# Kernel tuning notes

Hardware: AMD Instinct MI355X
Metric: run time of the kernel (lower is better)

## Reference

```python
import jax, jax.numpy as jnp
import numpy as np

VOCAB, EDIM, WFEAT, LABELS, SLOPE = 50000, 128, 128, 2, 0.01
N = 8192

def setup_inputs() -> dict:
    key = jax.random.key(0)
    ks = jax.random.split(key, 8)
    inSen = jax.random.randint(ks[0], (N,), 0, VOCAB, dtype=jnp.int64) if jax.config.read('jax_enable_x64') else jax.random.randint(ks[0], (N,), 0, VOCAB, dtype=jnp.int32)
    adj = jax.random.randint(ks[1], (N, N), 0, 2, dtype=jnp.int32)
    emb = jax.random.normal(ks[2], (VOCAB, EDIM), dtype=jnp.float32)
    W = jax.random.normal(ks[3], (EDIM, WFEAT), dtype=jnp.float32) * (1.0 / np.sqrt(EDIM))
    a_src = jax.random.normal(ks[4], (WFEAT,), dtype=jnp.float32) * (1.0 / np.sqrt(WFEAT))
    a_dst = jax.random.normal(ks[5], (WFEAT,), dtype=jnp.float32) * (1.0 / np.sqrt(WFEAT))
    cls_W = jax.random.normal(ks[6], (WFEAT, LABELS), dtype=jnp.float32) * (1.0 / np.sqrt(WFEAT))
    cls_b = jax.random.normal(ks[7], (LABELS,), dtype=jnp.float32) * 0.01
    return {"inSen": inSen, "adj": adj, "selfLink": 1, "emb": emb, "W": W,
            "a_src": a_src, "a_dst": a_dst, "cls_W": cls_W, "cls_b": cls_b}

def reference(inSen, adj, selfLink, emb, W, a_src, a_dst, cls_W, cls_b):
    # Embedding lookup: (N, edim)
    words = emb[inSen]
    # GAT layer: linear projection then adjacency-masked additive attention
    h = words @ W                              # (N, wFeat)
    f_src = h @ a_src                          # (N,)
    f_dst = h @ a_dst                          # (N,)
    e = jax.nn.leaky_relu(f_src[:, None] + f_dst[None, :], negative_slope=SLOPE)  # (N, N)
    mask = (adj + selfLink * jnp.eye(adj.shape[0], dtype=adj.dtype)) > 0
    e = jnp.where(mask, e, jnp.float32(-1e9))
    attention = jax.nn.softmax(e, axis=1)      # (N, N)
    sentence = attention @ h                   # (N, wFeat)
    # Max pool over words, classify
    poolSentence = jnp.max(sentence, axis=0)   # (wFeat,)
    label = jax.nn.softmax(poolSentence @ cls_W + cls_b, axis=0)  # (labels,)
    return (poolSentence, attention, sentence, label)
```

## Files before the change

kernel.cpp:

```cpp
#include <hip/hip_runtime.h>
#include <hip/hip_bf16.h>

#define NR 8192
#define WF 128

typedef short bf16x8 __attribute__((ext_vector_type(8)));
typedef float f32x4 __attribute__((ext_vector_type(4)));

static __device__ __forceinline__ unsigned int f2bf(float f) {
    unsigned int u = __float_as_uint(f);
    return (u + 0x7fffu + ((u >> 16) & 1u)) >> 16;
}
static __device__ __forceinline__ void atomicMaxF(float* addr, float v) {
    if (v >= 0.f) atomicMax((int*)addr, __float_as_int(v));
    else          atomicMin((unsigned int*)addr, __float_as_uint(v));
}
static __device__ __forceinline__ float lrelu(float x) { return x > 0.f ? x : 0.01f * x; }

__global__ __launch_bounds__(256) void k_proj(
    const int* __restrict__ inSen, const float* __restrict__ emb,
    const float* __restrict__ W, const float* __restrict__ a_src,
    const float* __restrict__ a_dst, float* __restrict__ f_src,
    float* __restrict__ f_dst, float* __restrict__ maxfd,
    unsigned short* __restrict__ hB)
{
    __shared__ float ht[16 * 132];
    const int t = threadIdx.x;
    const int f = t & 127, rh = t >> 7;
    const int i0 = blockIdx.x * 16;

    int wd[8];
    #pragma unroll
    for (int r = 0; r < 8; ++r) wd[r] = inSen[i0 + rh * 8 + r];
    float h[8];
    #pragma unroll
    for (int r = 0; r < 8; ++r) h[r] = 0.f;

    for (int k4 = 0; k4 < 32; ++k4) {
        const float w0 = W[(k4 * 4 + 0) * WF + f];
        const float w1 = W[(k4 * 4 + 1) * WF + f];
        const float w2 = W[(k4 * 4 + 2) * WF + f];
        const float w3 = W[(k4 * 4 + 3) * WF + f];
        #pragma unroll
        for (int r = 0; r < 8; ++r) {
            float4 ev = ((const float4*)(emb + (size_t)wd[r] * 128))[k4];
            h[r] += ev.x * w0 + ev.y * w1 + ev.z * w2 + ev.w * w3;
        }
    }
    #pragma unroll
    for (int r = 0; r < 8; ++r) ht[(rh * 8 + r) * 132 + f] = h[r];
    __syncthreads();

    if (t < 16) {
        float s = 0.f, d = 0.f;
        for (int k4 = 0; k4 < 32; ++k4) {
            float4 hv = *(const float4*)(ht + t * 132 + k4 * 4);
            float4 as = ((const float4*)a_src)[k4];
            float4 ad = ((const float4*)a_dst)[k4];
            s += hv.x * as.x + hv.y * as.y + hv.z * as.z + hv.w * as.w;
            d += hv.x * ad.x + hv.y * ad.y + hv.z * ad.z + hv.w * ad.w;
        }
        f_src[i0 + t] = s;
        f_dst[i0 + t] = d;
        float dm = d;
        #pragma unroll
        for (int o = 1; o < 16; o <<= 1) dm = fmaxf(dm, __shfl_xor(dm, o));
        if (t == 0) atomicMaxF(maxfd, dm);
    }
    {
        const int kb = blockIdx.x >> 1, half = blockIdx.x & 1;
        const int nf = t >> 5, l32 = t & 31;
        const int qloc = l32 >> 4, fx = l32 & 15;
        const int lane = (half * 2 + qloc) * 16 + fx;
        const float* hp = ht + (qloc * 8) * 132 + nf * 16 + fx;
        uint4 v;
        v.x = f2bf(hp[0 * 132]) | (f2bf(hp[1 * 132]) << 16);
        v.y = f2bf(hp[2 * 132]) | (f2bf(hp[3 * 132]) << 16);
        v.z = f2bf(hp[4 * 132]) | (f2bf(hp[5 * 132]) << 16);
        v.w = f2bf(hp[6 * 132]) | (f2bf(hp[7 * 132]) << 16);
        *(uint4*)(hB + ((size_t)kb * 8 + nf) * 512 + lane * 8) = v;
    }
}

static __device__ __forceinline__ void adj_chunk(
    int c, int4 a, const float* __restrict__ fdl, int lane, int row, int sl,
    float fs, float C, int shl,
    unsigned int* __restrict__ mrow, float& sum)
{
    const float4 f = *(const float4*)(fdl + c * 256 + 4 * lane);
    const bool m0 = a.x > 0, m1 = a.y > 0, m2 = a.z > 0, m3 = a.w > 0;
    float p0 = m0 ? __expf(lrelu(fs + f.x) - C) : 0.f;
    float p1 = m1 ? __expf(lrelu(fs + f.y) - C) : 0.f;
    float p2 = m2 ? __expf(lrelu(fs + f.z) - C) : 0.f;
    float p3 = m3 ? __expf(lrelu(fs + f.w) - C) : 0.f;
    unsigned int nib = (m0 ? 1u : 0u) | (m1 ? 2u : 0u) | (m2 ? 4u : 0u) | (m3 ? 8u : 0u);
    float ssum = p0 + p1 + p2 + p3;
    if (c == (row >> 8)) {
        if (lane == ((row & 255) >> 2)) {
            const int jd = row & 3;
            const int aj = jd == 0 ? a.x : jd == 1 ? a.y : jd == 2 ? a.z : a.w;
            const float fj = jd == 0 ? f.x : jd == 1 ? f.y : jd == 2 ? f.z : f.w;
            const bool mo = aj > 0, mn = (aj + sl) > 0;
            if (mn != mo) {
                const float pd = __expf(lrelu(fs + fj) - C);
                if (mn) { nib |= 1u << jd; ssum += pd; }
                else    { nib &= ~(1u << jd); ssum -= pd; }
            }
        }
    }
    sum += ssum;
    unsigned int v = nib << shl;
    v |= __shfl_xor(v, 1);
    v |= __shfl_xor(v, 2);
    v |= __shfl_xor(v, 4);
    if ((lane & 7) == 0) mrow[c * 8 + (lane >> 3)] = v;
}

__global__ __launch_bounds__(256, 4) void k_adj(
    const int* __restrict__ adj, const int* __restrict__ slP,
    const float* __restrict__ f_src, const float* __restrict__ f_dst,
    const float* __restrict__ maxfd, unsigned int* __restrict__ maskG,
    float* __restrict__ invl)
{
    __shared__ float fdl[NR];
    const int t = threadIdx.x, lane = t & 63, w = t >> 6;
    const int row = blockIdx.x * 4 + w;
    const int sl = slP[0];
    const int* __restrict__ ap = adj + (size_t)row * NR + 4 * lane;

    int4 a0 = *(const int4*)(ap + 0 * 256);
    int4 a1 = *(const int4*)(ap + 1 * 256);
    int4 a2 = *(const int4*)(ap + 2 * 256);
    int4 a3 = *(const int4*)(ap + 3 * 256);
    int4 a4 = *(const int4*)(ap + 4 * 256);
    int4 a5 = *(const int4*)(ap + 5 * 256);
    int4 a6 = *(const int4*)(ap + 6 * 256);
    int4 a7 = *(const int4*)(ap + 7 * 256);

    #pragma unroll
    for (int i = 0; i < 8; ++i)
        *(float4*)(fdl + (i * 256 + t) * 4) = *(const float4*)(f_dst + (i * 256 + t) * 4);

    const float fs = f_src[row];
    const float C = lrelu(fs + maxfd[0]);
    unsigned int* __restrict__ mrow = maskG + (size_t)row * 256;
    const int shl = 4 * (lane & 7);
    float sum = 0.f;
    __syncthreads();

    #define ADJC(c, reg) adj_chunk((c), (reg), fdl, lane, row, sl, fs, C, shl, mrow, sum)
    #pragma unroll 1
    for (int g = 0; g < 24; g += 8) {
        ADJC(g + 0, a0); a0 = *(const int4*)(ap + (g +  8) * 256);
        ADJC(g + 1, a1); a1 = *(const int4*)(ap + (g +  9) * 256);
        ADJC(g + 2, a2); a2 = *(const int4*)(ap + (g + 10) * 256);
        ADJC(g + 3, a3); a3 = *(const int4*)(ap + (g + 11) * 256);
        ADJC(g + 4, a4); a4 = *(const int4*)(ap + (g + 12) * 256);
        ADJC(g + 5, a5); a5 = *(const int4*)(ap + (g + 13) * 256);
        ADJC(g + 6, a6); a6 = *(const int4*)(ap + (g + 14) * 256);
        ADJC(g + 7, a7); a7 = *(const int4*)(ap + (g + 15) * 256);
    }
    ADJC(24, a0); ADJC(25, a1); ADJC(26, a2); ADJC(27, a3);
    ADJC(28, a4); ADJC(29, a5); ADJC(30, a6); ADJC(31, a7);
    #undef ADJC

    #pragma unroll
    for (int o = 1; o < 64; o <<= 1) sum += __shfl_xor(sum, o);
    if (lane == 0) invl[row] = 1.0f / sum;
}

__global__ __launch_bounds__(512, 4) void k_att(
    const unsigned int* __restrict__ maskG, const float* __restrict__ f_src,
    const float* __restrict__ f_dst, const float* __restrict__ maxfd,
    const float* __restrict__ invl, const unsigned short* __restrict__ hB,
    float* __restrict__ att, float* __restrict__ sent)
{
    __shared__ float red[8][2048];
    const int t = threadIdx.x;
    const int lane = t & 63, w = t >> 6;
    const int strip = blockIdx.x;
    const int i0 = strip * 16;
    const int fx = lane & 15, quad = lane >> 4;
    const int row = i0 + fx;
    const float fs = f_src[row];
    const float C = lrelu(fs + maxfd[0]);
    const float il = invl[row];
    float* __restrict__ ar = att + (size_t)row * NR;
    const unsigned int* __restrict__ mrow = maskG + (size_t)row * 256;
    f32x4 acc[8] = {};
    const int kb0 = w * 32;
    const unsigned short* __restrict__ hp0 = hB + (size_t)kb0 * 4096 + lane * 8;
    const float* __restrict__ fp0 = f_dst + kb0 * 32 + quad * 8;

    uint4 mw = *(const uint4*)(mrow + kb0);
    float4 fdA0 = *(const float4*)(fp0);
    float4 fdA1 = *(const float4*)(fp0 + 4);

    #pragma unroll 1
    for (int g = 0; g < 8; ++g) {
        uint4 mw_n;
        if (g < 7) mw_n = *(const uint4*)(mrow + kb0 + (g + 1) * 4);
        #pragma unroll
        for (int j = 0; j < 4; ++j) {
            const int i = g * 4 + j;
            const unsigned short* hp = hp0 + (size_t)i * 4096;
            bf16x8 bfr[8];
            #pragma unroll
            for (int nf = 0; nf < 8; ++nf) bfr[nf] = *(const bf16x8*)(hp + nf * 512);
            float4 fdB0, fdB1;
            {
                const float* fpn = fp0 + (i + 1) * 32;
                fdB0 = *(const float4*)(fpn);
                fdB1 = *(const float4*)(fpn + 4);
            }
            const unsigned int mword = (j == 0) ? mw.x : (j == 1) ? mw.y
                                     : (j == 2) ? mw.z : mw.w;
            const unsigned int mbyte = (mword >> (quad * 8)) & 0xffu;
            const float fv[8] = {fdA0.x, fdA0.y, fdA0.z, fdA0.w,
                                 fdA1.x, fdA1.y, fdA1.z, fdA1.w};
            float p[8];
            #pragma unroll
            for (int jj = 0; jj < 8; ++jj)
                p[jj] = ((mbyte >> jj) & 1u) ? __expf(lrelu(fs + fv[jj]) - C) : 0.f;

            const int kk = (kb0 + i) * 32;
            const float4 w0 = make_float4(p[0] * il, p[1] * il, p[2] * il, p[3] * il);
            const float4 w1 = make_float4(p[4] * il, p[5] * il, p[6] * il, p[7] * il);
            *(float4*)(ar + kk + quad * 8) = w0;
            *(float4*)(ar + kk + quad * 8 + 4) = w1;

            union { uint4 u; bf16x8 v; } cv;
            cv.u.x = f2bf(p[0]) | (f2bf(p[1]) << 16);
            cv.u.y = f2bf(p[2]) | (f2bf(p[3]) << 16);
            cv.u.z = f2bf(p[4]) | (f2bf(p[5]) << 16);
            cv.u.w = f2bf(p[6]) | (f2bf(p[7]) << 16);
            #pragma unroll
            for (int nf = 0; nf < 8; ++nf)
                acc[nf] = __builtin_amdgcn_mfma_f32_16x16x32_bf16(cv.v, bfr[nf], acc[nf], 0, 0, 0);
            fdA0 = fdB0; fdA1 = fdB1;
        }
        if (g < 7) mw = mw_n;
    }
    #pragma unroll
    for (int reg = 0; reg < 4; ++reg) {
        #pragma unroll
        for (int nf = 0; nf < 8; ++nf)
            red[w][(quad * 4 + reg) * 128 + nf * 16 + fx] = acc[nf][reg];
    }
    __syncthreads();
    {
        const int e0 = t * 4;
        const int m = e0 >> 7, f0 = e0 & 127;
        const float vin = invl[i0 + m];
        float vv[4];
        #pragma unroll
        for (int j = 0; j < 4; ++j) {
            float s = 0.f;
            #pragma unroll
            for (int sx = 0; sx < 8; ++sx) s += red[sx][e0 + j];
            vv[j] = s * vin;
        }
        *(float4*)(sent + (size_t)(i0 + m) * WF + f0) = make_float4(vv[0], vv[1], vv[2], vv[3]);
    }
}

__global__ __launch_bounds__(256) void k_pool(
    const float* __restrict__ sent, float* __restrict__ partial)
{
    __shared__ float s[256];
    const int t = threadIdx.x;
    const int f = t & 127, rh = t >> 7;
    const int r0 = blockIdx.x * 32;
    float m = -1e30f;
    #pragma unroll
    for (int j = 0; j < 16; ++j)
        m = fmaxf(m, sent[(size_t)(r0 + j * 2 + rh) * WF + f]);
    s[t] = m;
    __syncthreads();
    if (t < 128) partial[blockIdx.x * 128 + t] = fmaxf(s[t], s[t + 128]);
}

__global__ __launch_bounds__(128) void k_label(
    const float* __restrict__ partial, const float* __restrict__ cls_W,
    const float* __restrict__ cls_b, float* __restrict__ pool,
    float* __restrict__ label)
{
    __shared__ float s0[128], s1[128];
    const int t = threadIdx.x;
    float m = -1e30f;
    for (int b = 0; b < 256; ++b) m = fmaxf(m, partial[b * 128 + t]);
    pool[t] = m;
    s0[t] = m * cls_W[t * 2 + 0];
    s1[t] = m * cls_W[t * 2 + 1];
    __syncthreads();
    if (t == 0) {
        float z0 = cls_b[0], z1 = cls_b[1];
        for (int f = 0; f < 128; ++f) { z0 += s0[f]; z1 += s1[f]; }
        float mm = fmaxf(z0, z1);
        float e0 = __expf(z0 - mm), e1 = __expf(z1 - mm);
        float inv = 1.0f / (e0 + e1);
        label[0] = e0 * inv;
        label[1] = e1 * inv;
    }
}

extern "C" void kernel_launch(void* const* d_in, const int* in_sizes, int n_in,
                              void* d_out, int out_size, void* d_ws, size_t ws_size,
                              hipStream_t stream)
{
    const int*   inSen    = (const int*)d_in[0];
    const int*   adj      = (const int*)d_in[1];
    const int*   selfLink = (const int*)d_in[2];
    const float* emb      = (const float*)d_in[3];
    const float* W        = (const float*)d_in[4];
    const float* a_src    = (const float*)d_in[5];
    const float* a_dst    = (const float*)d_in[6];
    const float* cls_W    = (const float*)d_in[7];
    const float* cls_b    = (const float*)d_in[8];

    float* out   = (float*)d_out;
    float* pool  = out;
    float* att   = out + 128;
    float* sent  = att + (size_t)NR * NR;
    float* label = sent + (size_t)NR * WF;

    char* ws = (char*)d_ws;
    unsigned short* hB    = (unsigned short*)ws;
    unsigned int*   maskG = (unsigned int*)(ws + (2u << 20));
    float* f_src   = (float*)(ws + (10u << 20));
    float* f_dst   = f_src + NR;
    float* invl    = f_dst + NR;
    float* maxfd   = invl + NR;
    float* partial = maxfd + 64;

    hipMemsetAsync(maxfd, 0xFF, 4, stream);
    k_proj<<<NR / 16, 256, 0, stream>>>(inSen, emb, W, a_src, a_dst, f_src, f_dst, maxfd, hB);
    k_adj<<<NR / 4, 256, 0, stream>>>(adj, selfLink, f_src, f_dst, maxfd, maskG, invl);
    k_att<<<NR / 16, 512, 0, stream>>>(maskG, f_src, f_dst, maxfd, invl, hB, att, sent);
    k_pool<<<NR / 32, 256, 0, stream>>>(sent, partial);
    k_label<<<1, 128, 0, stream>>>(partial, cls_W, cls_b, pool, label);
}
```

Before: 626.0 us.

## Fuse max-pool into attention kernel and stage f_dst in shared memory

The attention kernel now copies the whole f_dst vector into its shared reduction buffer at the start and reads it from there, replacing the per-step global float4 prefetches. Its main loop is rewritten as a simpler strided loop that drops the manual software pipelining of mask words and f_dst values. After writing each strip of sentence rows, the kernel reduces a per-strip column max in shared memory and writes it to the partial buffer, which removes the separate pool kernel and its re-read of sentence. The label kernel now reduces 512 partials with four independent accumulators. The cost is an extra barrier, and loads that were previously prefetched are no longer explicitly overlapped with compute.

After: 596.0 us. 4.8% less time.

```diff
diff --git a/kernel.cpp b/kernel.cpp
--- a/kernel.cpp
+++ b/kernel.cpp
@@ -173,57 +173,51 @@
     const unsigned int* __restrict__ maskG, const float* __restrict__ f_src,
     const float* __restrict__ f_dst, const float* __restrict__ maxfd,
     const float* __restrict__ invl, const unsigned short* __restrict__ hB,
-    float* __restrict__ att, float* __restrict__ sent)
+    float* __restrict__ att, float* __restrict__ sent, float* __restrict__ partial)
 {
     __shared__ float red[8][2048];
+    float* fdl = &red[0][0];
     const int t = threadIdx.x;
     const int lane = t & 63, w = t >> 6;
     const int strip = blockIdx.x;
     const int i0 = strip * 16;
     const int fx = lane & 15, quad = lane >> 4;
     const int row = i0 + fx;
+
+    #pragma unroll
+    for (int i = 0; i < 4; ++i)
+        *(float4*)(fdl + (i * 512 + t) * 4) = *(const float4*)(f_dst + (i * 512 + t) * 4);
+
     const float fs = f_src[row];
     const float C = lrelu(fs + maxfd[0]);
     const float il = invl[row];
     float* __restrict__ ar = att + (size_t)row * NR;
     const unsigned int* __restrict__ mrow = maskG + (size_t)row * 256;
     f32x4 acc[8] = {};
-    const int kb0 = w * 32;
-    const unsigned short* __restrict__ hp0 = hB + (size_t)kb0 * 4096 + lane * 8;
-    const float* __restrict__ fp0 = f_dst + kb0 * 32 + quad * 8;
-
-    uint4 mw = *(const uint4*)(mrow + kb0);
-    float4 fdA0 = *(const float4*)(fp0);
-    float4 fdA1 = *(const float4*)(fp0 + 4);
-
-    #pragma unroll 1
-    for (int g = 0; g < 8; ++g) {
-        uint4 mw_n;
-        if (g < 7) mw_n = *(const uint4*)(mrow + kb0 + (g + 1) * 4);
-        #pragma unroll
-        for (int j = 0; j < 4; ++j) {
-            const int i = g * 4 + j;
-            const unsigned short* hp = hp0 + (size_t)i * 4096;
+    const int k0 = w * 1024;
+    __syncthreads();
+
+    for (int kk4 = k0; kk4 < k0 + 1024; kk4 += 128) {
+        const uint4 mw = *(const uint4*)(mrow + (kk4 >> 5));
+        const unsigned int mwa[4] = {mw.x, mw.y, mw.z, mw.w};
+        #pragma unroll
+        for (int j4 = 0; j4 < 4; ++j4) {
+            const int kk = kk4 + j4 * 32;
+            const int kb = kk >> 5;
+            const unsigned short* hp = hB + (size_t)kb * 4096 + lane * 8;
             bf16x8 bfr[8];
             #pragma unroll
             for (int nf = 0; nf < 8; ++nf) bfr[nf] = *(const bf16x8*)(hp + nf * 512);
-            float4 fdB0, fdB1;
-            {
-                const float* fpn = fp0 + (i + 1) * 32;
-                fdB0 = *(const float4*)(fpn);
-                fdB1 = *(const float4*)(fpn + 4);
-            }
-            const unsigned int mword = (j == 0) ? mw.x : (j == 1) ? mw.y
-                                     : (j == 2) ? mw.z : mw.w;
-            const unsigned int mbyte = (mword >> (quad * 8)) & 0xffu;
-            const float fv[8] = {fdA0.x, fdA0.y, fdA0.z, fdA0.w,
-                                 fdA1.x, fdA1.y, fdA1.z, fdA1.w};
+
+            const unsigned int mbyte = (mwa[j4] >> (quad * 8)) & 0xffu;
+            const float4 fd0 = *(const float4*)(fdl + kk + quad * 8);
+            const float4 fd1 = *(const float4*)(fdl + kk + quad * 8 + 4);
+            const float fv[8] = {fd0.x, fd0.y, fd0.z, fd0.w, fd1.x, fd1.y, fd1.z, fd1.w};
             float p[8];
             #pragma unroll
-            for (int jj = 0; jj < 8; ++jj)
-                p[jj] = ((mbyte >> jj) & 1u) ? __expf(lrelu(fs + fv[jj]) - C) : 0.f;
-
-            const int kk = (kb0 + i) * 32;
+            for (int j = 0; j < 8; ++j)
+                p[j] = ((mbyte >> j) & 1u) ? __expf(lrelu(fs + fv[j]) - C) : 0.f;
+
             const float4 w0 = make_float4(p[0] * il, p[1] * il, p[2] * il, p[3] * il);
             const float4 w1 = make_float4(p[4] * il, p[5] * il, p[6] * il, p[7] * il);
             *(float4*)(ar + kk + quad * 8) = w0;
@@ -237,10 +231,9 @@
             #pragma unroll
             for (int nf = 0; nf < 8; ++nf)
                 acc[nf] = __builtin_amdgcn_mfma_f32_16x16x32_bf16(cv.v, bfr[nf], acc[nf], 0, 0, 0);
-            fdA0 = fdB0; fdA1 = fdB1;
-        }
-        if (g < 7) mw = mw_n;
-    }
+        }
+    }
+    __syncthreads();
     #pragma unroll
     for (int reg = 0; reg < 4; ++reg) {
         #pragma unroll
@@ -248,9 +241,9 @@
             red[w][(quad * 4 + reg) * 128 + nf * 16 + fx] = acc[nf][reg];
     }
     __syncthreads();
+    const int e0 = t * 4;
+    const int m = e0 >> 7, f0 = e0 & 127;
     {
-        const int e0 = t * 4;
-        const int m = e0 >> 7, f0 = e0 & 127;
         const float vin = invl[i0 + m];
         float vv[4];
         #pragma unroll
@@ -261,23 +254,16 @@
             vv[j] = s * vin;
         }
         *(float4*)(sent + (size_t)(i0 + m) * WF + f0) = make_float4(vv[0], vv[1], vv[2], vv[3]);
-    }
-}
-
-__global__ __launch_bounds__(256) void k_pool(
-    const float* __restrict__ sent, float* __restrict__ partial)
-{
-    __shared__ float s[256];
-    const int t = threadIdx.x;
-    const int f = t & 127, rh = t >> 7;
-    const int r0 = blockIdx.x * 32;
-    float m = -1e30f;
-    #pragma unroll
-    for (int j = 0; j < 16; ++j)
-        m = fmaxf(m, sent[(size_t)(r0 + j * 2 + rh) * WF + f]);
-    s[t] = m;
-    __syncthreads();
-    if (t < 128) partial[blockIdx.x * 128 + t] = fmaxf(s[t], s[t + 128]);
+        red[0][e0 + 0] = vv[0]; red[0][e0 + 1] = vv[1];
+        red[0][e0 + 2] = vv[2]; red[0][e0 + 3] = vv[3];
+    }
+    __syncthreads();
+    if (t < 128) {
+        float mx = red[0][t];
+        #pragma unroll
+        for (int mm = 1; mm < 16; ++mm) mx = fmaxf(mx, red[0][mm * 128 + t]);
+        partial[strip * 128 + t] = mx;
+    }
 }
 
 __global__ __launch_bounds__(128) void k_label(
@@ -287,8 +273,14 @@
 {
     __shared__ float s0[128], s1[128];
     const int t = threadIdx.x;
-    float m = -1e30f;
-    for (int b = 0; b < 256; ++b) m = fmaxf(m, partial[b * 128 + t]);
+    float m0 = -1e30f, m1 = -1e30f, m2 = -1e30f, m3 = -1e30f;
+    for (int b = 0; b < 512; b += 4) {
+        m0 = fmaxf(m0, partial[(b + 0) * 128 + t]);
+        m1 = fmaxf(m1, partial[(b + 1) * 128 + t]);
+        m2 = fmaxf(m2, partial[(b + 2) * 128 + t]);
+        m3 = fmaxf(m3, partial[(b + 3) * 128 + t]);
+    }
+    const float m = fmaxf(fmaxf(m0, m1), fmaxf(m2, m3));
     pool[t] = m;
     s0[t] = m * cls_W[t * 2 + 0];
     s1[t] = m * cls_W[t * 2 + 1];
@@ -336,7 +328,6 @@
     hipMemsetAsync(maxfd, 0xFF, 4, stream);
     k_proj<<<NR / 16, 256, 0, stream>>>(inSen, emb, W, a_src, a_dst, f_src, f_dst, maxfd, hB);
     k_adj<<<NR / 4, 256, 0, stream>>>(adj, selfLink, f_src, f_dst, maxfd, maskG, invl);
-    k_att<<<NR / 16, 512, 0, stream>>>(maskG, f_src, f_dst, maxfd, invl, hB, att, sent);
-    k_pool<<<NR / 32, 256, 0, stream>>>(sent, partial);
+    k_att<<<NR / 16, 512, 0, stream>>>(maskG, f_src, f_dst, maxfd, invl, hB, att, sent, partial);
     k_label<<<1, 128, 0, stream>>>(partial, cls_W, cls_b, pool, label);
 }
```
